# Performance work log

Hardware: AMD Instinct MI355X
Metric: run time of the kernel (lower is better)

Reference implementation:

```python
import jax, jax.numpy as jnp
import numpy as np

B, L, WIN = 65536, 240, 24
EMB_SZS = [(367, 20), (7, 4), (24, 8)]
N_CONT = 16
H1, H2, OUT_SZ = 512, 256, 24
N_EMB = sum(nf for _, nf in EMB_SZS)
NUM_WAVE = 6 * (WIN // 2) + 6 * (WIN // 4)  # 108


def pool_matrix(lin, w):
    # PyTorch AdaptiveAvgPool1d: bin i averages x[floor(i*lin/w) : ceil((i+1)*lin/w)]
    P = np.zeros((lin, w), np.float32)
    for i in range(w):
        s = (i * lin) // w
        e = -((-(i + 1) * lin) // w)
        P[s:e, i] = 1.0 / (e - s)
    return jnp.asarray(P)


def conv1(x, w, dil):
    # single-channel 1D cross-correlation, no bias; x: [B, Lin], w: [ks]
    ks = w.shape[0]
    lout = x.shape[-1] - dil * (ks - 1)
    return sum(w[k] * x[:, k * dil:k * dil + lout] for k in range(ks))


def branch(xw, wa, wb):
    # conv(ks, dil=1) -> adaptive_avg_pool(12) -> leaky_relu(0.1), then same with dil=2 -> pool(6)
    ca = conv1(xw, wa, 1)                                   # [B, L-ks+1]
    fa = jax.nn.leaky_relu(ca @ pool_matrix(ca.shape[-1], WIN // 2), 0.1)  # [B,12]
    cb = conv1(fa, wb, 2)                                   # [B, 12-2*(ks-1)]
    fb = jax.nn.leaky_relu(cb @ pool_matrix(cb.shape[-1], WIN // 4), 0.1)  # [B,6]
    return fa, fb


def setup_inputs() -> dict:
    key = jax.random.key(0)
    ks_list = list(range(1, 7))
    keys = jax.random.split(key, 32)
    d = {}
    d['x_window'] = jax.random.normal(keys[0], (B, 1, L), jnp.float32)
    cats = [jax.random.randint(jax.random.fold_in(keys[1], i), (B,), 0, ni)
            for i, (ni, _) in enumerate(EMB_SZS)]
    d['x_cat'] = jnp.stack(cats, axis=1).astype(jnp.int64)
    d['x_cont'] = jax.random.normal(keys[2], (B, N_CONT), jnp.float32)
    for i, ks in enumerate(ks_list):
        d[f'wk{ks}a'] = jax.random.normal(keys[3 + 2 * i], (ks,), jnp.float32) * 0.5
        d[f'wk{ks}b'] = jax.random.normal(keys[4 + 2 * i], (ks,), jnp.float32) * 0.5
    for i, (ni, nf) in enumerate(EMB_SZS):
        d[f'E{i}'] = jax.random.normal(keys[16 + i], (ni, nf), jnp.float32) * 0.01
    d['bn_g'] = jnp.ones((N_CONT,), jnp.float32)
    d['bn_b'] = jnp.zeros((N_CONT,), jnp.float32)
    n_in = N_EMB + N_CONT
    d['W1'] = jax.random.normal(keys[20], (n_in, H1), jnp.float32) * (1.0 / np.sqrt(n_in))
    d['b1'] = jnp.zeros((H1,), jnp.float32)
    d['W2'] = jax.random.normal(keys[21], (H1, H2), jnp.float32) * (1.0 / np.sqrt(H1))
    d['b2'] = jnp.zeros((H2,), jnp.float32)
    d['Wlin'] = jax.random.normal(keys[22], (NUM_WAVE + H2, OUT_SZ), jnp.float32) * (1.0 / np.sqrt(NUM_WAVE + H2))
    return d


def reference(x_window, x_cat, x_cont,
              wk1a, wk1b, wk2a, wk2b, wk3a, wk3b, wk4a, wk4b, wk5a, wk5b, wk6a, wk6b,
              E0, E1, E2, bn_g, bn_b, W1, b1, W2, b2, Wlin):
    xw = x_window[:, 0, :]  # [B, L]
    feats = []
    for wa, wb in [(wk1a, wk1b), (wk2a, wk2b), (wk3a, wk3b),
                   (wk4a, wk4b), (wk5a, wk5b), (wk6a, wk6b)]:
        fa, fb = branch(xw, wa, wb)
        feats += [fa, fb]
    ffc = jnp.concatenate(feats, axis=1)  # [B, 108]
    # embeddings
    emb = jnp.concatenate([E0[x_cat[:, 0]], E1[x_cat[:, 1]], E2[x_cat[:, 2]]], axis=1)  # [B, 32]
    # BatchNorm1d on continuous features (training-mode batch stats, eps=1e-5)
    m = jnp.mean(x_cont, axis=0)
    v = jnp.var(x_cont, axis=0)
    xc = (x_cont - m) / jnp.sqrt(v + 1e-5) * bn_g + bn_b
    x = jnp.concatenate([emb, xc], axis=1)  # [B, 48]
    x = jax.nn.relu(x @ W1 + b1)
    x = jax.nn.relu(x @ W2 + b2)  # [B, 256]
    fc = jnp.concatenate([ffc, x], axis=1)  # [B, 364]
    return fc @ Wlin  # [B, 24]
```

## Files before the change

### kernel.cpp

```cpp
#include <hip/hip_runtime.h>

typedef __bf16 bf16x8 __attribute__((ext_vector_type(8)));
typedef float  f32x4  __attribute__((ext_vector_type(4)));
typedef unsigned short ushort_t;

#define B_TOTAL 65536
#define NSTILE  4096

__device__ __forceinline__ ushort_t f2bf(float f) {
  unsigned u = __builtin_bit_cast(unsigned, f);
  u += 0x7fffu + ((u >> 16) & 1u);
  return (ushort_t)(u >> 16);
}
__device__ __forceinline__ unsigned pk2(float lo, float hi) {
  unsigned r;
  asm("v_cvt_pk_bf16_f32 %0, %1, %2" : "=v"(r) : "v"(lo), "v"(hi));
  return r;
}
__device__ __forceinline__ float lrelu(float v) { return v >= 0.f ? v : 0.1f * v; }
__device__ __forceinline__ int swzi(int row, int rb, int col) {
  return ((row * rb + col * 2) ^ ((row & 7) << 4)) >> 1;
}
__device__ __forceinline__ bf16x8 ld_frag(const ushort_t* p8) {
  return __builtin_bit_cast(bf16x8, *(const uint4*)p8);
}
__device__ __forceinline__ bf16x8 frag_swz(const ushort_t* base, int row, int rb, int kcol0) {
  int b = (row * rb + kcol0 * 2) ^ ((row & 7) << 4);
  return __builtin_bit_cast(bf16x8, *(const uint4*)((const char*)base + b));
}
__device__ __forceinline__ f32x4 mfma16(bf16x8 a, bf16x8 b, f32x4 c) {
  return __builtin_amdgcn_mfma_f32_16x16x32_bf16(a, b, c, 0, 0, 0);
}

__global__ __launch_bounds__(256) void bn_partial(const float* __restrict__ xc,
                                                  float* __restrict__ ws) {
  __shared__ float red[512];
  const int t = threadIdx.x;
  const int c = t & 15, g = t >> 4;
  const int r0 = blockIdx.x * 256;
  float s = 0.f, q = 0.f;
  for (int i = 0; i < 16; ++i) {
    float v = xc[(size_t)(r0 + g + i * 16) * 16 + c];
    s += v; q += v * v;
  }
  red[t] = s; red[256 + t] = q;
  __syncthreads();
  if (t < 16) {
    float ss = 0.f, qq = 0.f;
    for (int gg = 0; gg < 16; ++gg) { ss += red[gg * 16 + t]; qq += red[256 + gg * 16 + t]; }
    ws[blockIdx.x * 32 + t] = ss;
    ws[blockIdx.x * 32 + 16 + t] = qq;
  }
}

__global__ __launch_bounds__(256) void bn_final(const float* __restrict__ ws_in,
                                                float* __restrict__ ws_out,
                                                const float* __restrict__ g_,
                                                const float* __restrict__ b_) {
  __shared__ float red[512];
  const int t = threadIdx.x;
  const int c = t & 15, g = t >> 4;
  float s = 0.f, q = 0.f;
  for (int i = 0; i < 16; ++i) {
    int blk = g * 16 + i;
    s += ws_in[blk * 32 + c];
    q += ws_in[blk * 32 + 16 + c];
  }
  red[t] = s; red[256 + t] = q;
  __syncthreads();
  if (t < 16) {
    float ss = 0.f, qq = 0.f;
    for (int gg = 0; gg < 16; ++gg) { ss += red[gg * 16 + t]; qq += red[256 + gg * 16 + t]; }
    float mean  = ss / (float)B_TOTAL;
    float var   = qq / (float)B_TOTAL - mean * mean;
    float scale = g_[t] / sqrtf(var + 1e-5f);
    ws_out[8192 + t]      = scale;
    ws_out[8192 + 16 + t] = b_[t] - mean * scale;
  }
}

__global__ __launch_bounds__(256) void pack_weights(const float* __restrict__ W1,
                                                    const float* __restrict__ W2,
                                                    const float* __restrict__ Wl,
                                                    ushort_t* __restrict__ w1p,
                                                    ushort_t* __restrict__ w2p,
                                                    ushort_t* __restrict__ wlp) {
  int u = blockIdx.x * 256 + threadIdx.x;
  if (u < 32768) {
    int i = u & 7, lane = (u >> 3) & 63, kb = u >> 14;
    int k = kb * 32 + ((lane >> 4) << 3) + i;
    int n = (((u >> 9) & 31) << 4) + (lane & 15);
    w1p[u] = f2bf(k < 48 ? W1[k * 512 + n] : 0.f);
  } else if (u < 32768 + 131072) {
    int v = u - 32768;
    int i = v & 7, lane = (v >> 3) & 63, kb = v >> 13;
    int k = kb * 32 + ((lane >> 4) << 3) + i;
    int n = (((v >> 9) & 15) << 4) + (lane & 15);
    w2p[v] = f2bf(W2[k * 256 + n]);
  } else if (u < 32768 + 131072 + 12288) {
    int v = u - (32768 + 131072);
    int i = v & 7, lane = (v >> 3) & 63, kb = v >> 10;
    int k = kb * 32 + ((lane >> 4) << 3) + i;
    int n = (((v >> 9) & 1) << 4) + (lane & 15);
    float val = 0.f;
    if (n < 24) {
      if (k < 108)       val = Wl[k * 24 + n];
      else if (k >= 128) val = Wl[(k - 20) * 24 + n];
    }
    wlp[v] = f2bf(val);
  }
}

struct WkPtrs { const float* wk[12]; };

__global__ __launch_bounds__(256) void pack_conv(WkPtrs wp,
                                                 ushort_t* __restrict__ Apack,
                                                 ushort_t* __restrict__ Bpack) {
  int u = blockIdx.x * 256 + threadIdx.x;
  if (u < 20480) {
    int i = u & 7, lane = (u >> 3) & 63;
    int knt = u >> 9;
    int kb = knt / 5, nt = knt % 5;
    int k = kb * 32 + ((lane >> 4) << 3) + i;
    int n = nt * 16 + (lane & 15);
    float val = 0.f;
    if (n < 72 && k < 240) {
      int br = n / 12, ii = n - br * 12, ks = br + 1, lin = 240 - br;
      int si = ii * lin / 12, ei = ((ii + 1) * lin + 11) / 12;
      const float* wa = wp.wk[2 * br];
      float acc = 0.f;
      for (int kk = 0; kk < ks; ++kk) {
        int j = k - kk;
        if (j >= si && j < ei) acc += wa[kk];
      }
      val = acc / (float)(ei - si);
    }
    Apack[u] = f2bf(val);
  } else if (u < 20480 + 6144) {
    int v = u - 20480;
    int i = v & 7, lane = (v >> 3) & 63;
    int knt = v >> 9;
    int kb = knt / 3, nt = knt % 3;
    int kcol = kb * 32 + ((lane >> 4) << 3) + i;
    int n = nt * 16 + (lane & 15);
    float val = 0.f;
    if (n < 36 && kcol < 108) {
      int brk = kcol / 18, ii = kcol - brk * 18;
      int brn = n / 6, j = n - brn * 6;
      if (brk == brn && ii < 12) {
        int ks = brn + 1, lcb = 12 - 2 * brn;
        int sj = j * lcb / 6, ej = ((j + 1) * lcb + 5) / 6;
        const float* wb = wp.wk[2 * brn + 1];
        float acc = 0.f;
        for (int kk = 0; kk < ks; ++kk) {
          int q = ii - 2 * kk;
          if (q >= sj && q < ej) acc += wb[kk];
        }
        val = acc / (float)(ej - sj);
      }
    }
    Bpack[v] = f2bf(val);
  }
}

struct ConvParams {
  const float* xw;
  const ushort_t* Apack;
  const ushort_t* Bpack;
  ushort_t*    ffc;
};

__global__ __launch_bounds__(512, 6) void conv_kernel(ConvParams p) {
  __shared__ __align__(16) char smem[49152];
  ushort_t* s_xw = (ushort_t*)smem;
  ushort_t* s_fc = (ushort_t*)(smem + 32768);

  const int t = threadIdx.x, lane = t & 63, w = t >> 6;
  const int s0 = blockIdx.x * 64;
  const f32x4 fzero = {0.f, 0.f, 0.f, 0.f};

  for (int u = t; u < 1024; u += 512) ((uint4*)s_fc)[u] = uint4{0, 0, 0, 0};
  if (t < 128) {
    int r = t >> 1, m = t & 1;
    *(uint4*)((char*)s_xw + ((r * 512 + 480 + m * 16) ^ ((r & 7) << 4))) = uint4{0, 0, 0, 0};
  }
  for (int u = t; u < 64 * 60; u += 512) {
    int s = u / 60, m4 = u - s * 60;
    float4 v = *(const float4*)(p.xw + (size_t)(s0 + s) * 240 + 4 * m4);
    uint2 pkv; pkv.x = pk2(v.x, v.y); pkv.y = pk2(v.z, v.w);
    *(uint2*)((char*)s_xw + ((s * 512 + m4 * 8) ^ ((s & 7) << 4))) = pkv;
  }
  __syncthreads();

  auto do0a = [&](int nt, int st) {
    f32x4 acc = fzero;
    #pragma unroll
    for (int kb = 0; kb < 8; ++kb) {
      bf16x8 a = ld_frag(p.Apack + (size_t)((kb * 5 + nt) * 64 + lane) * 8);
      bf16x8 b = frag_swz(s_xw, st * 16 + (lane & 15), 512, kb * 32 + ((lane >> 4) << 3));
      acc = mfma16(a, b, acc);
    }
    int n0 = nt * 16 + ((lane >> 4) << 2);
    int br = n0 / 12;
    int col0 = n0 + 6 * br;
    int row = st * 16 + (lane & 15);
    unsigned lo = pk2(lrelu(acc[0]), lrelu(acc[1]));
    unsigned hi = pk2(lrelu(acc[2]), lrelu(acc[3]));
    *(unsigned*)((char*)s_fc + ((row * 256 + col0 * 2) ^ ((row & 7) << 4))) = lo;
    *(unsigned*)((char*)s_fc + ((row * 256 + (col0 + 2) * 2) ^ ((row & 7) << 4))) = hi;
  };
  do0a(w % 5, w / 5);
  do0a((w + 8) % 5, (w + 8) / 5);
  if (w < 4) do0a((w + 16) % 5, (w + 16) / 5);
  __syncthreads();

  const int nt0 = w % 3, st0 = w / 3;
  f32x4 accB0 = fzero, accB1 = fzero;
  #pragma unroll
  for (int kb = 0; kb < 4; ++kb) {
    bf16x8 a = ld_frag(p.Bpack + (size_t)((kb * 3 + nt0) * 64 + lane) * 8);
    bf16x8 b = frag_swz(s_fc, st0 * 16 + (lane & 15), 256, kb * 32 + ((lane >> 4) << 3));
    accB0 = mfma16(a, b, accB0);
  }
  const int nt1 = (w + 8) % 3, st1 = (w + 8) / 3;
  if (w < 4) {
    #pragma unroll
    for (int kb = 0; kb < 4; ++kb) {
      bf16x8 a = ld_frag(p.Bpack + (size_t)((kb * 3 + nt1) * 64 + lane) * 8);
      bf16x8 b = frag_swz(s_fc, st1 * 16 + (lane & 15), 256, kb * 32 + ((lane >> 4) << 3));
      accB1 = mfma16(a, b, accB1);
    }
  }
  __syncthreads();
  auto wr0b = [&](f32x4 acc, int nt, int st) {
    int n0 = nt * 16 + ((lane >> 4) << 2);
    if (n0 < 36) {
      int row = st * 16 + (lane & 15);
      int br0 = n0 / 6, c0 = n0 + 12 * (br0 + 1);
      int n2 = n0 + 2, br2 = n2 / 6, c2 = n2 + 12 * (br2 + 1);
      *(unsigned*)((char*)s_fc + ((row * 256 + c0 * 2) ^ ((row & 7) << 4))) =
          pk2(lrelu(acc[0]), lrelu(acc[1]));
      *(unsigned*)((char*)s_fc + ((row * 256 + c2 * 2) ^ ((row & 7) << 4))) =
          pk2(lrelu(acc[2]), lrelu(acc[3]));
    }
  };
  wr0b(accB0, nt0, st0);
  if (w < 4) wr0b(accB1, nt1, st1);
  __syncthreads();

  for (int u = t; u < 1024; u += 512) {
    int ln = u & 63, st = (u >> 6) & 3, kb = u >> 8;
    int row = st * 16 + (ln & 15);
    int colb = (kb * 32 + ((ln >> 4) << 3)) * 2;
    uint4 v = *(const uint4*)((const char*)s_fc + ((row * 256 + colb) ^ ((row & 7) << 4)));
    size_t stile = (size_t)blockIdx.x * 4 + st;
    *(uint4*)((char*)p.ffc + (((size_t)kb * NSTILE + stile) * 64 + ln) * 16) = v;
  }
}

struct MlpParams {
  const int*   xcat;
  const float* xcont;
  const float* E0; const float* E1; const float* E2;
  const float* b1; const float* b2;
  const ushort_t* w1p; const ushort_t* w2p; const ushort_t* wlp;
  const ushort_t* ffc;
  const float* stats;
  float*       out;
};

__global__ __launch_bounds__(512, 4) void mlp_kernel(MlpParams p) {
  __shared__ __align__(16) char smem[73856];
  ushort_t* s_h1  = (ushort_t*)smem;
  ushort_t* s_fc  = (ushort_t*)smem;
  ushort_t* s_x48 = (ushort_t*)(smem + 65536);
  float*    s_bn  = (float*)(smem + 73728);

  const int t    = threadIdx.x;
  const int lane = t & 63;
  const int w    = t >> 6;
  const int s0   = blockIdx.x * 64;
  const f32x4 fzero = {0.f, 0.f, 0.f, 0.f};

  if (t < 32) s_bn[t] = p.stats[t];
  for (int u = t; u < 64 * 16; u += 512) { int s = u >> 4; s_x48[swzi(s, 128, 48 + (u & 15))] = 0; }
  __syncthreads();

  for (int u = t; u < 64 * 48; u += 512) {
    int s = u / 48, c = u - s * 48, gs = s0 + s;
    float v;
    if (c < 20)      v = p.E0[(size_t)p.xcat[gs * 3 + 0] * 20 + c];
    else if (c < 24) v = p.E1[(size_t)p.xcat[gs * 3 + 1] * 4 + (c - 20)];
    else if (c < 32) v = p.E2[(size_t)p.xcat[gs * 3 + 2] * 8 + (c - 24)];
    else { int cc = c - 32; v = p.xcont[(size_t)gs * 16 + cc] * s_bn[cc] + s_bn[16 + cc]; }
    s_x48[swzi(s, 128, c)] = f2bf(v);
  }
  __syncthreads();

  {
    bf16x8 bx[4][2];
    #pragma unroll
    for (int st = 0; st < 4; ++st)
      #pragma unroll
      for (int kb = 0; kb < 2; ++kb)
        bx[st][kb] = frag_swz(s_x48, st * 16 + (lane & 15), 128, kb * 32 + ((lane >> 4) << 3));
    #pragma unroll
    for (int j = 0; j < 4; ++j) {
      int nt = w * 4 + j;
      bf16x8 a0 = ld_frag(p.w1p + (size_t)((0 * 32 + nt) * 64 + lane) * 8);
      bf16x8 a1 = ld_frag(p.w1p + (size_t)((1 * 32 + nt) * 64 + lane) * 8);
      f32x4 acc[4];
      #pragma unroll
      for (int st = 0; st < 4; ++st) {
        acc[st] = mfma16(a0, bx[st][0], fzero);
        acc[st] = mfma16(a1, bx[st][1], acc[st]);
      }
      int n0 = nt * 16 + ((lane >> 4) << 2);
      float4 bb = *(const float4*)(p.b1 + n0);
      #pragma unroll
      for (int st = 0; st < 4; ++st) {
        int row = st * 16 + (lane & 15);
        float v0 = fmaxf(acc[st][0] + bb.x, 0.f);
        float v1 = fmaxf(acc[st][1] + bb.y, 0.f);
        float v2 = fmaxf(acc[st][2] + bb.z, 0.f);
        float v3 = fmaxf(acc[st][3] + bb.w, 0.f);
        uint2 pkv; pkv.x = pk2(v0, v1); pkv.y = pk2(v2, v3);
        *(uint2*)((char*)s_h1 + ((row * 1024 + n0 * 2) ^ ((row & 7) << 4))) = pkv;
      }
    }
  }
  __syncthreads();

  {
    const int nt0 = w * 2;
    f32x4 acc[2][4];
    #pragma unroll
    for (int jm = 0; jm < 2; ++jm)
      #pragma unroll
      for (int st = 0; st < 4; ++st) acc[jm][st] = fzero;
    uint4 pa[2][2];
    pa[0][0] = *(const uint4*)(p.w2p + (size_t)((0 * 16 + nt0 + 0) * 64 + lane) * 8);
    pa[0][1] = *(const uint4*)(p.w2p + (size_t)((0 * 16 + nt0 + 1) * 64 + lane) * 8);
    pa[1][0] = *(const uint4*)(p.w2p + (size_t)((1 * 16 + nt0 + 0) * 64 + lane) * 8);
    pa[1][1] = *(const uint4*)(p.w2p + (size_t)((1 * 16 + nt0 + 1) * 64 + lane) * 8);
    #pragma unroll
    for (int kb = 0; kb < 16; ++kb) {
      bf16x8 a0 = __builtin_bit_cast(bf16x8, pa[kb & 1][0]);
      bf16x8 a1 = __builtin_bit_cast(bf16x8, pa[kb & 1][1]);
      if (kb < 14) {
        pa[kb & 1][0] = *(const uint4*)(p.w2p + (size_t)(((kb + 2) * 16 + nt0 + 0) * 64 + lane) * 8);
        pa[kb & 1][1] = *(const uint4*)(p.w2p + (size_t)(((kb + 2) * 16 + nt0 + 1) * 64 + lane) * 8);
      }
      #pragma unroll
      for (int st = 0; st < 4; ++st) {
        bf16x8 b = frag_swz(s_h1, st * 16 + (lane & 15), 1024, kb * 32 + ((lane >> 4) << 3));
        acc[0][st] = mfma16(a0, b, acc[0][st]);
        acc[1][st] = mfma16(a1, b, acc[1][st]);
      }
    }
    __syncthreads();
    #pragma unroll
    for (int jm = 0; jm < 2; ++jm) {
      int n0 = (nt0 + jm) * 16 + ((lane >> 4) << 2);
      float4 bb = *(const float4*)(p.b2 + n0);
      #pragma unroll
      for (int st = 0; st < 4; ++st) {
        int row = st * 16 + (lane & 15);
        float v0 = fmaxf(acc[jm][st][0] + bb.x, 0.f);
        float v1 = fmaxf(acc[jm][st][1] + bb.y, 0.f);
        float v2 = fmaxf(acc[jm][st][2] + bb.z, 0.f);
        float v3 = fmaxf(acc[jm][st][3] + bb.w, 0.f);
        uint2 pkv; pkv.x = pk2(v0, v1); pkv.y = pk2(v2, v3);
        *(uint2*)((char*)s_fc + ((row * 512 + n0 * 2) ^ ((row & 7) << 4))) = pkv;
      }
    }
  }
  __syncthreads();

  {
    const int st = w & 3, nt = w >> 2;
    const size_t stile = (size_t)blockIdx.x * 4 + st;
    f32x4 acc = fzero;
    #pragma unroll
    for (int kb = 0; kb < 12; ++kb) {
      bf16x8 a = ld_frag(p.wlp + (size_t)((kb * 2 + nt) * 64 + lane) * 8);
      bf16x8 b;
      if (kb < 4) b = ld_frag(p.ffc + (((size_t)kb * NSTILE + stile) * 64 + lane) * 8);
      else        b = frag_swz(s_fc, st * 16 + (lane & 15), 512, (kb - 4) * 32 + ((lane >> 4) << 3));
      acc = mfma16(a, b, acc);
    }
    int n0 = nt * 16 + ((lane >> 4) << 2);
    if (n0 < 24) {
      int sg = s0 + st * 16 + (lane & 15);
      *(float2*)(p.out + (size_t)sg * 24 + n0)     = make_float2(acc[0], acc[1]);
      *(float2*)(p.out + (size_t)sg * 24 + n0 + 2) = make_float2(acc[2], acc[3]);
    }
  }
}

extern "C" void kernel_launch(void* const* d_in, const int* in_sizes, int n_in,
                              void* d_out, int out_size, void* d_ws, size_t ws_size,
                              hipStream_t stream) {
  const float* xcont = (const float*)d_in[2];
  float* ws  = (float*)d_ws;
  char*  wsb = (char*)d_ws;
  ushort_t* w1p   = (ushort_t*)(wsb + 36864);
  ushort_t* w2p   = (ushort_t*)(wsb + 102400);
  ushort_t* wlp   = (ushort_t*)(wsb + 364544);
  ushort_t* Apack = (ushort_t*)(wsb + 389120);
  ushort_t* Bpack = (ushort_t*)(wsb + 430080);
  ushort_t* ffc   = (ushort_t*)(wsb + 524288);

  WkPtrs wp;
  for (int i = 0; i < 12; ++i) wp.wk[i] = (const float*)d_in[3 + i];
  pack_conv<<<104, 256, 0, stream>>>(wp, Apack, Bpack);

  ConvParams cp;
  cp.xw = (const float*)d_in[0];
  cp.Apack = Apack; cp.Bpack = Bpack;
  cp.ffc = ffc;
  conv_kernel<<<B_TOTAL / 64, 512, 0, stream>>>(cp);

  bn_partial<<<256, 256, 0, stream>>>(xcont, ws);
  bn_final<<<1, 256, 0, stream>>>(ws, ws, (const float*)d_in[18], (const float*)d_in[19]);
  pack_weights<<<688, 256, 0, stream>>>((const float*)d_in[20], (const float*)d_in[22],
                                        (const float*)d_in[24], w1p, w2p, wlp);

  MlpParams p;
  p.xcat  = (const int*)d_in[1];
  p.xcont = xcont;
  p.E0 = (const float*)d_in[15]; p.E1 = (const float*)d_in[16]; p.E2 = (const float*)d_in[17];
  p.b1 = (const float*)d_in[21]; p.b2 = (const float*)d_in[23];
  p.w1p = w1p; p.w2p = w2p; p.wlp = wlp; p.ffc = ffc;
  p.stats = ws + 8192;
  p.out = (float*)d_out;
  mlp_kernel<<<B_TOTAL / 64, 512, 0, stream>>>(p);
}
```

Measured before the change: 69.66 us.

## Split H1 into two halves to shrink LDS and raise MLP kernel occupancy

```diff
diff --git a/kernel.cpp b/kernel.cpp
--- a/kernel.cpp
+++ b/kernel.cpp
@@ -269,12 +269,11 @@
   float*       out;
 };
 
-__global__ __launch_bounds__(512, 4) void mlp_kernel(MlpParams p) {
-  __shared__ __align__(16) char smem[73856];
+__global__ __launch_bounds__(512, 6) void mlp_kernel(MlpParams p) {
+  __shared__ __align__(16) char smem[40960];
   ushort_t* s_h1  = (ushort_t*)smem;
   ushort_t* s_fc  = (ushort_t*)smem;
-  ushort_t* s_x48 = (ushort_t*)(smem + 65536);
-  float*    s_bn  = (float*)(smem + 73728);
+  ushort_t* s_x48 = (ushort_t*)(smem + 32768);
 
   const int t    = threadIdx.x;
   const int lane = t & 63;
@@ -282,41 +281,51 @@
   const int s0   = blockIdx.x * 64;
   const f32x4 fzero = {0.f, 0.f, 0.f, 0.f};
 
-  if (t < 32) s_bn[t] = p.stats[t];
+  const int nt2 = w * 2;
+  uint4 pa[2][2];
+  pa[0][0] = *(const uint4*)(p.w2p + (size_t)((0 * 16 + nt2 + 0) * 64 + lane) * 8);
+  pa[0][1] = *(const uint4*)(p.w2p + (size_t)((0 * 16 + nt2 + 1) * 64 + lane) * 8);
+  pa[1][0] = *(const uint4*)(p.w2p + (size_t)((1 * 16 + nt2 + 0) * 64 + lane) * 8);
+  pa[1][1] = *(const uint4*)(p.w2p + (size_t)((1 * 16 + nt2 + 1) * 64 + lane) * 8);
+
   for (int u = t; u < 64 * 16; u += 512) { int s = u >> 4; s_x48[swzi(s, 128, 48 + (u & 15))] = 0; }
-  __syncthreads();
-
   for (int u = t; u < 64 * 48; u += 512) {
     int s = u / 48, c = u - s * 48, gs = s0 + s;
     float v;
     if (c < 20)      v = p.E0[(size_t)p.xcat[gs * 3 + 0] * 20 + c];
     else if (c < 24) v = p.E1[(size_t)p.xcat[gs * 3 + 1] * 4 + (c - 20)];
     else if (c < 32) v = p.E2[(size_t)p.xcat[gs * 3 + 2] * 8 + (c - 24)];
-    else { int cc = c - 32; v = p.xcont[(size_t)gs * 16 + cc] * s_bn[cc] + s_bn[16 + cc]; }
+    else { int cc = c - 32; v = p.xcont[(size_t)gs * 16 + cc] * p.stats[cc] + p.stats[16 + cc]; }
     s_x48[swzi(s, 128, c)] = f2bf(v);
   }
-  __syncthreads();
-
-  {
-    bf16x8 bx[4][2];
-    #pragma unroll
-    for (int st = 0; st < 4; ++st)
-      #pragma unroll
-      for (int kb = 0; kb < 2; ++kb)
-        bx[st][kb] = frag_swz(s_x48, st * 16 + (lane & 15), 128, kb * 32 + ((lane >> 4) << 3));
-    #pragma unroll
-    for (int j = 0; j < 4; ++j) {
-      int nt = w * 4 + j;
-      bf16x8 a0 = ld_frag(p.w1p + (size_t)((0 * 32 + nt) * 64 + lane) * 8);
-      bf16x8 a1 = ld_frag(p.w1p + (size_t)((1 * 32 + nt) * 64 + lane) * 8);
+
+  f32x4 acc2[2][4];
+  #pragma unroll
+  for (int jm = 0; jm < 2; ++jm)
+    #pragma unroll
+    for (int st = 0; st < 4; ++st) acc2[jm][st] = fzero;
+  uint4 fbf[4];
+
+  __syncthreads();
+
+  #pragma unroll
+  for (int h = 0; h < 2; ++h) {
+    #pragma unroll
+    for (int j = 0; j < 2; ++j) {
+      int ntp = w * 2 + j;
+      int gnt = h * 16 + ntp;
+      bf16x8 a0 = ld_frag(p.w1p + (size_t)((0 * 32 + gnt) * 64 + lane) * 8);
+      bf16x8 a1 = ld_frag(p.w1p + (size_t)((1 * 32 + gnt) * 64 + lane) * 8);
       f32x4 acc[4];
       #pragma unroll
       for (int st = 0; st < 4; ++st) {
-        acc[st] = mfma16(a0, bx[st][0], fzero);
-        acc[st] = mfma16(a1, bx[st][1], acc[st]);
-      }
-      int n0 = nt * 16 + ((lane >> 4) << 2);
-      float4 bb = *(const float4*)(p.b1 + n0);
+        bf16x8 bx0 = frag_swz(s_x48, st * 16 + (lane & 15), 128, 0 + ((lane >> 4) << 3));
+        bf16x8 bx1 = frag_swz(s_x48, st * 16 + (lane & 15), 128, 32 + ((lane >> 4) << 3));
+        acc[st] = mfma16(a0, bx0, fzero);
+        acc[st] = mfma16(a1, bx1, acc[st]);
+      }
+      int n0l = ntp * 16 + ((lane >> 4) << 2);
+      float4 bb = *(const float4*)(p.b1 + h * 256 + n0l);
       #pragma unroll
       for (int st = 0; st < 4; ++st) {
         int row = st * 16 + (lane & 15);
@@ -325,67 +334,65 @@
         float v2 = fmaxf(acc[st][2] + bb.z, 0.f);
         float v3 = fmaxf(acc[st][3] + bb.w, 0.f);
         uint2 pkv; pkv.x = pk2(v0, v1); pkv.y = pk2(v2, v3);
-        *(uint2*)((char*)s_h1 + ((row * 1024 + n0 * 2) ^ ((row & 7) << 4))) = pkv;
-      }
-    }
-  }
-  __syncthreads();
-
-  {
-    const int nt0 = w * 2;
-    f32x4 acc[2][4];
-    #pragma unroll
-    for (int jm = 0; jm < 2; ++jm)
+        *(uint2*)((char*)s_h1 + ((row * 512 + n0l * 2) ^ ((row & 7) << 4))) = pkv;
+      }
+    }
+    __syncthreads();
+
+    if (h == 1) {
+      const int st3 = w & 3;
+      const size_t stile = (size_t)blockIdx.x * 4 + st3;
       #pragma unroll
-      for (int st = 0; st < 4; ++st) acc[jm][st] = fzero;
-    uint4 pa[2][2];
-    pa[0][0] = *(const uint4*)(p.w2p + (size_t)((0 * 16 + nt0 + 0) * 64 + lane) * 8);
-    pa[0][1] = *(const uint4*)(p.w2p + (size_t)((0 * 16 + nt0 + 1) * 64 + lane) * 8);
-    pa[1][0] = *(const uint4*)(p.w2p + (size_t)((1 * 16 + nt0 + 0) * 64 + lane) * 8);
-    pa[1][1] = *(const uint4*)(p.w2p + (size_t)((1 * 16 + nt0 + 1) * 64 + lane) * 8);
-    #pragma unroll
-    for (int kb = 0; kb < 16; ++kb) {
+      for (int kb = 0; kb < 4; ++kb)
+        fbf[kb] = *(const uint4*)((const char*)p.ffc +
+                    (((size_t)kb * NSTILE + stile) * 64 + lane) * 16);
+    }
+
+    #pragma unroll
+    for (int kk = 0; kk < 8; ++kk) {
+      int kb = h * 8 + kk;
       bf16x8 a0 = __builtin_bit_cast(bf16x8, pa[kb & 1][0]);
       bf16x8 a1 = __builtin_bit_cast(bf16x8, pa[kb & 1][1]);
-      if (kb < 14) {
-        pa[kb & 1][0] = *(const uint4*)(p.w2p + (size_t)(((kb + 2) * 16 + nt0 + 0) * 64 + lane) * 8);
-        pa[kb & 1][1] = *(const uint4*)(p.w2p + (size_t)(((kb + 2) * 16 + nt0 + 1) * 64 + lane) * 8);
+      int kpre = kb + 2;
+      if (kpre < 16) {
+        pa[kb & 1][0] = *(const uint4*)(p.w2p + (size_t)((kpre * 16 + nt2 + 0) * 64 + lane) * 8);
+        pa[kb & 1][1] = *(const uint4*)(p.w2p + (size_t)((kpre * 16 + nt2 + 1) * 64 + lane) * 8);
       }
       #pragma unroll
       for (int st = 0; st < 4; ++st) {
-        bf16x8 b = frag_swz(s_h1, st * 16 + (lane & 15), 1024, kb * 32 + ((lane >> 4) << 3));
-        acc[0][st] = mfma16(a0, b, acc[0][st]);
-        acc[1][st] = mfma16(a1, b, acc[1][st]);
+        bf16x8 b = frag_swz(s_h1, st * 16 + (lane & 15), 512, kk * 32 + ((lane >> 4) << 3));
+        acc2[0][st] = mfma16(a0, b, acc2[0][st]);
+        acc2[1][st] = mfma16(a1, b, acc2[1][st]);
       }
     }
     __syncthreads();
-    #pragma unroll
-    for (int jm = 0; jm < 2; ++jm) {
-      int n0 = (nt0 + jm) * 16 + ((lane >> 4) << 2);
-      float4 bb = *(const float4*)(p.b2 + n0);
-      #pragma unroll
-      for (int st = 0; st < 4; ++st) {
-        int row = st * 16 + (lane & 15);
-        float v0 = fmaxf(acc[jm][st][0] + bb.x, 0.f);
-        float v1 = fmaxf(acc[jm][st][1] + bb.y, 0.f);
-        float v2 = fmaxf(acc[jm][st][2] + bb.z, 0.f);
-        float v3 = fmaxf(acc[jm][st][3] + bb.w, 0.f);
-        uint2 pkv; pkv.x = pk2(v0, v1); pkv.y = pk2(v2, v3);
-        *(uint2*)((char*)s_fc + ((row * 512 + n0 * 2) ^ ((row & 7) << 4))) = pkv;
-      }
+  }
+
+  #pragma unroll
+  for (int jm = 0; jm < 2; ++jm) {
+    int n0 = (nt2 + jm) * 16 + ((lane >> 4) << 2);
+    float4 bb = *(const float4*)(p.b2 + n0);
+    #pragma unroll
+    for (int st = 0; st < 4; ++st) {
+      int row = st * 16 + (lane & 15);
+      float v0 = fmaxf(acc2[jm][st][0] + bb.x, 0.f);
+      float v1 = fmaxf(acc2[jm][st][1] + bb.y, 0.f);
+      float v2 = fmaxf(acc2[jm][st][2] + bb.z, 0.f);
+      float v3 = fmaxf(acc2[jm][st][3] + bb.w, 0.f);
+      uint2 pkv; pkv.x = pk2(v0, v1); pkv.y = pk2(v2, v3);
+      *(uint2*)((char*)s_fc + ((row * 512 + n0 * 2) ^ ((row & 7) << 4))) = pkv;
     }
   }
   __syncthreads();
 
   {
     const int st = w & 3, nt = w >> 2;
-    const size_t stile = (size_t)blockIdx.x * 4 + st;
     f32x4 acc = fzero;
     #pragma unroll
     for (int kb = 0; kb < 12; ++kb) {
       bf16x8 a = ld_frag(p.wlp + (size_t)((kb * 2 + nt) * 64 + lane) * 8);
       bf16x8 b;
-      if (kb < 4) b = ld_frag(p.ffc + (((size_t)kb * NSTILE + stile) * 64 + lane) * 8);
+      if (kb < 4) b = __builtin_bit_cast(bf16x8, fbf[kb]);
       else        b = frag_swz(s_fc, st * 16 + (lane & 15), 512, (kb - 4) * 32 + ((lane >> 4) << 3));
       acc = mfma16(a, b, acc);
     }
```

New measurement: 103.1 us. 1.48x slower.
